# Performance work log

Hardware: AMD Instinct MI355X
Metric: run time of the kernel (lower is better)

Reference implementation:

```python
import jax, jax.numpy as jnp
import numpy as np

TOP_K = 2
EPS = 1e-6

def setup_inputs() -> dict:
    key = jax.random.key(0)
    ks = jax.random.split(key, 4)
    B, L, D, E, ED = 2, 2048, 2048, 8, 2048
    scale_gu = (6.0 / D) ** 0.5   # kaiming_uniform-ish bound
    scale_dn = (6.0 / ED) ** 0.5
    return {
        "x": jax.random.normal(ks[0], (B, L, D), jnp.float32),
        "router_scale": jnp.ones((D,), jnp.float32),
        "gate_w": jax.random.normal(ks[1], (D, E), jnp.float32) * (D ** -0.5),
        "gate_up": jax.random.uniform(ks[2], (E, D, 2 * ED), jnp.float32, -scale_gu, scale_gu),
        "down": jax.random.uniform(ks[3], (E, ED, D), jnp.float32, -scale_dn, scale_dn),
        "per_expert_scale": jnp.ones((E,), jnp.float32),
    }

def reference(x, router_scale, gate_w, gate_up, down, per_expert_scale):
    B, L, D = x.shape
    E = gate_up.shape[0]
    # --- Router: RMSNorm (no scale) * D^-0.5 * router_scale -> linear -> softmax -> topk -> renorm
    h = x * jax.lax.rsqrt(jnp.mean(x * x, axis=-1, keepdims=True) + EPS)
    h = h * (D ** -0.5) * router_scale
    logits = (h @ gate_w).astype(jnp.float32)            # [B,L,E]
    probs = jax.nn.softmax(logits, axis=-1)
    w, idx = jax.lax.top_k(probs, TOP_K)                 # [B,L,K]
    w = w / jnp.clip(jnp.sum(w, axis=-1, keepdims=True), 1e-12)
    w = w.astype(x.dtype)
    # --- Experts: dense compute over all experts, weighted combine by routing
    N = B * L
    xf = x.reshape(N, D)
    idxf = idx.reshape(N, TOP_K)
    wf = w.reshape(N, TOP_K)
    # combine[n,e] = sum_k wf[n,k] * (idxf[n,k]==e); top_k indices are distinct per token
    combine = jnp.zeros((N, E), x.dtype).at[jnp.arange(N)[:, None], idxf].add(wf)
    hh = jnp.einsum('nd,edf->nef', xf, gate_up)          # [N,E,2*ED]
    gate, up = jnp.split(hh, 2, axis=-1)
    act = jax.nn.gelu(gate, approximate=False) * up      # [N,E,ED]
    y = jnp.einsum('nef,efd->ned', act, down)            # [N,E,D]
    out = jnp.einsum('ne,ned->nd', combine * per_expert_scale, y)
    return out.reshape(B, L, D)
```

## Files before the change

### kernel.cpp

```cpp
#include <hip/hip_runtime.h>
#include <hip/hip_bf16.h>
#include <math.h>

#define NTOK 4096
#define DM   2048
#define NE   8
#define BM   128
#define BK   64

using f32x4  = float __attribute__((ext_vector_type(4)));
using bf16x8 = __bf16 __attribute__((ext_vector_type(8)));
using u32x4  = unsigned int __attribute__((ext_vector_type(4)));

__device__ __forceinline__ unsigned short bf16bits(float f){
  unsigned u = __builtin_bit_cast(unsigned, f);
  return (unsigned short)((u + 0x7fffu + ((u >> 16) & 1u)) >> 16);
}

__device__ __forceinline__ void load_lds16(const void* g, void* l){
  __builtin_amdgcn_global_load_lds(
      (const __attribute__((address_space(1))) unsigned int*)g,
      (__attribute__((address_space(3))) unsigned int*)l, 16, 0, 0);
}

__global__ __launch_bounds__(256) void router_kernel(
    const float* __restrict__ x, const float* __restrict__ rs,
    const float* __restrict__ gw, const float* __restrict__ pes,
    unsigned short* __restrict__ xbf, int* __restrict__ cnt,
    int* __restrict__ toklist, float* __restrict__ slotw)
{
  const int wv = threadIdx.x >> 6, l = threadIdx.x & 63;
  const int n = blockIdx.x * 4 + wv;
  const float* xr = x + (size_t)n * DM;
  unsigned short* xb = xbf + (size_t)n * DM;
  float ssq = 0.f;
  float lg[8] = {0,0,0,0,0,0,0,0};
  #pragma unroll
  for (int q = 0; q < 8; ++q){
    int c4 = l + 64 * q;
    float4 v = ((const float4*)xr)[c4];
    float4 r = ((const float4*)rs)[c4];
    ssq += v.x*v.x + v.y*v.y + v.z*v.z + v.w*v.w;
    ushort4 o; o.x = bf16bits(v.x); o.y = bf16bits(v.y); o.z = bf16bits(v.z); o.w = bf16bits(v.w);
    ((ushort4*)xb)[c4] = o;
    float xs0 = v.x*r.x, xs1 = v.y*r.y, xs2 = v.z*r.z, xs3 = v.w*r.w;
    const float4* gp = (const float4*)(gw + (size_t)c4 * 32);
    float4 ga, gb;
    ga = gp[0]; gb = gp[1];
    lg[0]+=xs0*ga.x; lg[1]+=xs0*ga.y; lg[2]+=xs0*ga.z; lg[3]+=xs0*ga.w;
    lg[4]+=xs0*gb.x; lg[5]+=xs0*gb.y; lg[6]+=xs0*gb.z; lg[7]+=xs0*gb.w;
    ga = gp[2]; gb = gp[3];
    lg[0]+=xs1*ga.x; lg[1]+=xs1*ga.y; lg[2]+=xs1*ga.z; lg[3]+=xs1*ga.w;
    lg[4]+=xs1*gb.x; lg[5]+=xs1*gb.y; lg[6]+=xs1*gb.z; lg[7]+=xs1*gb.w;
    ga = gp[4]; gb = gp[5];
    lg[0]+=xs2*ga.x; lg[1]+=xs2*ga.y; lg[2]+=xs2*ga.z; lg[3]+=xs2*ga.w;
    lg[4]+=xs2*gb.x; lg[5]+=xs2*gb.y; lg[6]+=xs2*gb.z; lg[7]+=xs2*gb.w;
    ga = gp[6]; gb = gp[7];
    lg[0]+=xs3*ga.x; lg[1]+=xs3*ga.y; lg[2]+=xs3*ga.z; lg[3]+=xs3*ga.w;
    lg[4]+=xs3*gb.x; lg[5]+=xs3*gb.y; lg[6]+=xs3*gb.z; lg[7]+=xs3*gb.w;
  }
  #pragma unroll
  for (int off = 32; off; off >>= 1){
    ssq += __shfl_xor(ssq, off, 64);
    #pragma unroll
    for (int e2 = 0; e2 < 8; ++e2) lg[e2] += __shfl_xor(lg[e2], off, 64);
  }
  if (l == 0){
    float c = rsqrtf(ssq * (1.0f/DM) + 1e-6f) * 0.022097086912079608f;
    float mx = -1e30f;
    #pragma unroll
    for (int e2 = 0; e2 < 8; ++e2){ lg[e2] *= c; mx = fmaxf(mx, lg[e2]); }
    float l0 = lg[0]; int i0 = 0;
    #pragma unroll
    for (int e2 = 1; e2 < 8; ++e2) if (lg[e2] > l0){ l0 = lg[e2]; i0 = e2; }
    int i1 = (i0 == 0) ? 1 : 0; float l1 = (i0 == 0) ? lg[1] : lg[0];
    #pragma unroll
    for (int e2 = 0; e2 < 8; ++e2){ if (e2 != i0 && lg[e2] > l1){ l1 = lg[e2]; i1 = e2; } }
    float p0 = expf(l0 - mx), p1 = expf(l1 - mx);
    float sw = fmaxf(p0 + p1, 1e-12f);
    float w0 = p0 / sw, w1 = p1 / sw;
    int s0 = atomicAdd(&cnt[i0], 1);
    toklist[i0 * NTOK + s0] = n;
    slotw[i0 * NTOK + s0] = w0 * pes[i0];
    int s1 = atomicAdd(&cnt[i1], 1);
    toklist[i1 * NTOK + s1] = n;
    slotw[i1 * NTOK + s1] = w1 * pes[i1];
  }
}

__global__ void scan_kernel(const int* __restrict__ cnt, int* __restrict__ basep){
  if (threadIdx.x == 0){
    int a = 0;
    for (int e = 0; e < NE; ++e){ basep[e] = a; a += cnt[e]; }
  }
}

__global__ __launch_bounds__(256) void conv_transpose_kernel(
    const float* __restrict__ W, unsigned short* __restrict__ Wt, int ncols)
{
  const int z = blockIdx.z;
  const float* src = W + (size_t)z * 2048 * ncols;
  unsigned short* dst = Wt + (size_t)z * ncols * 2048;
  const int n0 = blockIdx.x * 64, k0 = blockIdx.y * 64;
  __shared__ __align__(16) unsigned short t[64][72];
  const int tid = threadIdx.x;
  const int kl = tid >> 4;
  const int nl = (tid & 15) * 4;
  #pragma unroll
  for (int q = 0; q < 4; ++q){
    int k = kl + q * 16;
    float4 v = *(const float4*)(src + (size_t)(k0 + k) * ncols + n0 + nl);
    t[nl+0][k] = bf16bits(v.x);
    t[nl+1][k] = bf16bits(v.y);
    t[nl+2][k] = bf16bits(v.z);
    t[nl+3][k] = bf16bits(v.w);
  }
  __syncthreads();
  const int nr = tid >> 3;
  const int k8 = (tid & 7) * 8;
  #pragma unroll
  for (int q = 0; q < 2; ++q){
    int n = nr + q * 32;
    u32x4 v = *(const u32x4*)&t[n][k8];
    *(u32x4*)(dst + (size_t)(n0 + n) * 2048 + k0 + k8) = v;
  }
}

template<int MODE>
__global__ __launch_bounds__(256, MODE ? 3 : 2) void moe_gemm(
    const unsigned short* __restrict__ Abuf,
    const unsigned short* __restrict__ Wt,
    unsigned short* __restrict__ act,
    float* __restrict__ out,
    const int* __restrict__ cnt,
    const int* __restrict__ basep,
    const int* __restrict__ toklist,
    const float* __restrict__ slotw,
    int e0)
{
  constexpr int NH = (MODE == 0) ? 2 : 1;
  constexpr int BCOLS = NH * 128;
  const int z = blockIdx.z;
  const int e = e0 + z;
  const int ce = cnt[e];
  const int m0 = blockIdx.y * BM;
  if (m0 >= ce) return;
  const int fb = blockIdx.x * 128;
  const int tid = threadIdx.x;
  const int l = tid & 63;
  const int wv = tid >> 6;
  const int wr = wv >> 1, wc = wv & 1;
  const int baseE = basep[e];
  const size_t ncols = (MODE == 0) ? 4096 : 2048;
  const unsigned short* Wz = Wt + (size_t)z * ncols * 2048;

  __shared__ __align__(16) unsigned short As[BM * BK];
  __shared__ __align__(16) unsigned short Bs[BCOLS * BK];

  const unsigned short* asrc[4];
  #pragma unroll
  for (int q = 0; q < 4; ++q){
    int row = q * 32 + (tid >> 3);
    int g = (tid & 7) ^ (row & 7);
    long rs;
    if (MODE == 0) rs = toklist[e * NTOK + min(m0 + row, ce - 1)];
    else           rs = baseE + min(m0 + row, ce - 1);
    asrc[q] = Abuf + (size_t)rs * 2048 + g * 8;
  }
  const unsigned short* bsrc[NH * 4];
  #pragma unroll
  for (int q = 0; q < NH * 4; ++q){
    int col = q * 32 + (tid >> 3);
    int g = (tid & 7) ^ (col & 7);
    int n;
    if (MODE == 0) n = (col & 128) ? (2048 + fb + (col - 128)) : (fb + col);
    else           n = fb + col;
    bsrc[q] = Wz + (size_t)n * 2048 + g * 8;
  }

  f32x4 acc[NH][4][4];
  #pragma unroll
  for (int h = 0; h < NH; ++h)
    #pragma unroll
    for (int i = 0; i < 4; ++i)
      #pragma unroll
      for (int j = 0; j < 4; ++j)
        acc[h][i][j] = (f32x4){0.f, 0.f, 0.f, 0.f};

  const int aoff0 = (wr * 64 + (l & 15)) * BK;
  const int boff0 = (wc * 64 + (l & 15)) * BK;
  const int lsw = l & 7;
  const int lq = l >> 4;

  #pragma unroll 1
  for (int k0 = 0; k0 < 2048; k0 += BK){
    if (k0) __syncthreads();
    #pragma unroll
    for (int q = 0; q < 4; ++q)
      load_lds16(asrc[q] + k0, &As[q * 2048 + wv * 512]);
    #pragma unroll
    for (int q = 0; q < NH * 4; ++q)
      load_lds16(bsrc[q] + k0, &Bs[q * 2048 + wv * 512]);
    __syncthreads();
    #pragma unroll
    for (int kk = 0; kk < 2; ++kk){
      const int gsw = ((kk * 4 + lq) ^ lsw) * 8;
      bf16x8 af[4];
      #pragma unroll
      for (int mi = 0; mi < 4; ++mi)
        af[mi] = *(const bf16x8*)&As[aoff0 + mi * 16 * BK + gsw];
      #pragma unroll
      for (int h = 0; h < NH; ++h)
        #pragma unroll
        for (int ni = 0; ni < 4; ++ni){
          bf16x8 bfr = *(const bf16x8*)&Bs[boff0 + (h * 128 + ni * 16) * BK + gsw];
          #pragma unroll
          for (int mi = 0; mi < 4; ++mi)
            acc[h][mi][ni] = __builtin_amdgcn_mfma_f32_16x16x32_bf16(
                af[mi], bfr, acc[h][mi][ni], 0, 0, 0);
        }
    }
  }

  if (MODE == 0){
    const int fcol = fb + wc * 64 + (l & 15);
    #pragma unroll
    for (int mi = 0; mi < 4; ++mi)
      #pragma unroll
      for (int j = 0; j < 4; ++j){
        int s = m0 + wr * 64 + mi * 16 + lq * 4 + j;
        if (s < ce){
          size_t rowb = (size_t)(baseE + s) * 2048 + fcol;
          #pragma unroll
          for (int ni = 0; ni < 4; ++ni){
            float g = acc[0][mi][ni][j];
            float u = acc[1][mi][ni][j];
            float a = 0.5f * g * (1.0f + erff(g * 0.70710678118654752f)) * u;
            act[rowb + ni * 16] = bf16bits(a);
          }
        }
      }
  } else {
    #pragma unroll
    for (int mi = 0; mi < 4; ++mi)
      #pragma unroll
      for (int j = 0; j < 4; ++j){
        int s = m0 + wr * 64 + mi * 16 + lq * 4 + j;
        if (s < ce){
          int tokn = toklist[e * NTOK + s];
          float wgt = slotw[e * NTOK + s];
          float* orow = out + (size_t)tokn * 2048 + fb + wc * 64 + (l & 15);
          #pragma unroll
          for (int ni = 0; ni < 4; ++ni)
            atomicAdd(&orow[ni * 16], wgt * acc[0][mi][ni][j]);
        }
      }
  }
}

extern "C" void kernel_launch(void* const* d_in, const int* in_sizes, int n_in,
                              void* d_out, int out_size, void* d_ws, size_t ws_size,
                              hipStream_t stream)
{
  const float* x   = (const float*)d_in[0];
  const float* rs  = (const float*)d_in[1];
  const float* gw  = (const float*)d_in[2];
  const float* w1  = (const float*)d_in[3];
  const float* w2  = (const float*)d_in[4];
  const float* pes = (const float*)d_in[5];
  float* out = (float*)d_out;

  char* ws = (char*)d_ws;
  int*   cnt     = (int*)ws;
  int*   basep   = (int*)(ws + 64);
  int*   toklist = (int*)(ws + 256);
  float* slotw   = (float*)(ws + 256 + (size_t)NE * NTOK * 4);
  unsigned short* xbf = (unsigned short*)(ws + 256 + 2 * (size_t)NE * NTOK * 4);
  unsigned short* act = xbf + (size_t)NTOK * DM;
  unsigned short* wtb = act + (size_t)2 * NTOK * DM;

  const size_t fixed = (size_t)((char*)wtb - ws);
  const size_t per_e = (size_t)4096 * 2048 * 2;
  int EG = NE;
  while (EG > 1 && fixed + (size_t)EG * per_e > ws_size) EG >>= 1;

  hipMemsetAsync(d_out, 0, (size_t)out_size * sizeof(float), stream);
  hipMemsetAsync(cnt, 0, 64, stream);
  router_kernel<<<NTOK / 4, 256, 0, stream>>>(x, rs, gw, pes, xbf, cnt, toklist, slotw);
  scan_kernel<<<1, 64, 0, stream>>>(cnt, basep);

  for (int g = 0; g < NE; g += EG){
    conv_transpose_kernel<<<dim3(64, 32, EG), 256, 0, stream>>>(
        w1 + (size_t)g * 2048 * 4096, wtb, 4096);
    moe_gemm<0><<<dim3(16, 32, EG), 256, 0, stream>>>(
        xbf, wtb, act, out, cnt, basep, toklist, slotw, g);
  }
  for (int g = 0; g < NE; g += EG){
    conv_transpose_kernel<<<dim3(32, 32, EG), 256, 0, stream>>>(
        w2 + (size_t)g * 2048 * 2048, wtb, 2048);
    moe_gemm<1><<<dim3(16, 32, EG), 256, 0, stream>>>(
        act, wtb, act, out, cnt, basep, toklist, slotw, g);
  }
}
```

Baseline: 540.5 us.

## Rewrite MoE GEMM as 256x256 tile, 8-wave, 4-stage LDS pipeline

The MoE expert GEMM moves from 128-row tiles and 256 threads to 256x256 output tiles with 512 threads (8 waves). It uses a 4-buffer LDS ring with BK=32, prefetching three stages ahead via global_load_lds, with split barriers and s_setprio around the MFMA bursts. Gate and up columns are interleaved per 32-column group so each wave holds both halves for the GELU epilogue. The aim is to hide global-load latency and raise operand reuse per LDS byte, at the cost of higher register pressure, fewer blocks and more wasted rows when an expert's token count is not a multiple of 256.

```diff
diff --git a/kernel.cpp b/kernel.cpp
--- a/kernel.cpp
+++ b/kernel.cpp
@@ -5,8 +5,10 @@
 #define NTOK 4096
 #define DM   2048
 #define NE   8
-#define BM   128
-#define BK   64
+#define BK2  32
+#define NT   64
+#define TILE_BYTES 32768
+#define B_OFF      16384
 
 using f32x4  = float __attribute__((ext_vector_type(4)));
 using bf16x8 = __bf16 __attribute__((ext_vector_type(8)));
@@ -127,7 +129,7 @@
 }
 
 template<int MODE>
-__global__ __launch_bounds__(256, MODE ? 3 : 2) void moe_gemm(
+__global__ __launch_bounds__(512, 2) void moe_gemm(
     const unsigned short* __restrict__ Abuf,
     const unsigned short* __restrict__ Wt,
     unsigned short* __restrict__ act,
@@ -138,121 +140,148 @@
     const float* __restrict__ slotw,
     int e0)
 {
-  constexpr int NH = (MODE == 0) ? 2 : 1;
-  constexpr int BCOLS = NH * 128;
-  const int z = blockIdx.z;
-  const int e = e0 + z;
+  const int z = blockIdx.z, e = e0 + z;
   const int ce = cnt[e];
-  const int m0 = blockIdx.y * BM;
+  const int m0 = blockIdx.y * 256;
   if (m0 >= ce) return;
-  const int fb = blockIdx.x * 128;
+  const int fb = blockIdx.x * (MODE == 0 ? 128 : 256);
   const int tid = threadIdx.x;
   const int l = tid & 63;
   const int wv = tid >> 6;
-  const int wr = wv >> 1, wc = wv & 1;
+  const int wr = wv >> 2;
+  const int wc = wv & 3;
   const int baseE = basep[e];
   const size_t ncols = (MODE == 0) ? 4096 : 2048;
   const unsigned short* Wz = Wt + (size_t)z * ncols * 2048;
 
-  __shared__ __align__(16) unsigned short As[BM * BK];
-  __shared__ __align__(16) unsigned short Bs[BCOLS * BK];
-
-  const unsigned short* asrc[4];
-  #pragma unroll
-  for (int q = 0; q < 4; ++q){
-    int row = q * 32 + (tid >> 3);
-    int g = (tid & 7) ^ (row & 7);
-    long rs;
-    if (MODE == 0) rs = toklist[e * NTOK + min(m0 + row, ce - 1)];
-    else           rs = baseE + min(m0 + row, ce - 1);
-    asrc[q] = Abuf + (size_t)rs * 2048 + g * 8;
-  }
-  const unsigned short* bsrc[NH * 4];
-  #pragma unroll
-  for (int q = 0; q < NH * 4; ++q){
-    int col = q * 32 + (tid >> 3);
-    int g = (tid & 7) ^ (col & 7);
+  __shared__ __align__(16) unsigned short smem[4 * TILE_BYTES / 2];
+
+  const unsigned short* asrc[2];
+  #pragma unroll
+  for (int q = 0; q < 2; ++q){
+    int r = q * 128 + (tid >> 2);
+    int g = (tid & 3) ^ ((r >> 1) & 3);
+    long rsrc;
+    if (MODE == 0) rsrc = toklist[e * NTOK + min(m0 + r, ce - 1)];
+    else           rsrc = baseE + min(m0 + r, ce - 1);
+    asrc[q] = Abuf + (size_t)rsrc * 2048 + g * 8;
+  }
+  const unsigned short* bsrc[2];
+  #pragma unroll
+  for (int q = 0; q < 2; ++q){
+    int col = q * 128 + (tid >> 2);
+    int g = (tid & 3) ^ ((col >> 1) & 3);
     int n;
-    if (MODE == 0) n = (col & 128) ? (2048 + fb + (col - 128)) : (fb + col);
-    else           n = fb + col;
+    if (MODE == 0){ int sub = col & 63; n = fb + (col >> 6) * 32 + (sub & 31) + ((sub & 32) ? 2048 : 0); }
+    else n = fb + col;
     bsrc[q] = Wz + (size_t)n * 2048 + g * 8;
   }
-
-  f32x4 acc[NH][4][4];
-  #pragma unroll
-  for (int h = 0; h < NH; ++h)
-    #pragma unroll
-    for (int i = 0; i < 4; ++i)
-      #pragma unroll
-      for (int j = 0; j < 4; ++j)
-        acc[h][i][j] = (f32x4){0.f, 0.f, 0.f, 0.f};
-
-  const int aoff0 = (wr * 64 + (l & 15)) * BK;
-  const int boff0 = (wc * 64 + (l & 15)) * BK;
-  const int lsw = l & 7;
-  const int lq = l >> 4;
+  const int ldst = tid * 16;
+
+  const int kq = l >> 4;
+  const int swz = (kq ^ (((l & 15) >> 1) & 3)) * 16;
+  const int abase = (wr * 128 + (l & 15)) * 64 + swz;
+  const int bbase = B_OFF + (wc * 64 + (l & 15)) * 64 + swz;
+
+  f32x4 acc[8][4];
+  #pragma unroll
+  for (int i = 0; i < 8; ++i)
+    #pragma unroll
+    for (int j = 0; j < 4; ++j)
+      acc[i][j] = (f32x4){0.f, 0.f, 0.f, 0.f};
+
+  auto stage_a = [&](int buf, int st){
+    char* base = (char*)smem + buf * TILE_BYTES;
+    load_lds16(asrc[0] + st * BK2, base + ldst);
+    load_lds16(asrc[1] + st * BK2, base + 8192 + ldst);
+  };
+  auto stage_b = [&](int buf, int st){
+    char* base = (char*)smem + buf * TILE_BYTES + B_OFF;
+    load_lds16(bsrc[0] + st * BK2, base + ldst);
+    load_lds16(bsrc[1] + st * BK2, base + 8192 + ldst);
+  };
+
+  stage_a(0, 0); stage_b(0, 0);
+  stage_a(1, 1); stage_b(1, 1);
+  stage_a(2, 2); stage_b(2, 2);
+  asm volatile("s_waitcnt vmcnt(8)" ::: "memory");
+  __builtin_amdgcn_s_barrier();
+  asm volatile("" ::: "memory");
 
   #pragma unroll 1
-  for (int k0 = 0; k0 < 2048; k0 += BK){
-    if (k0) __syncthreads();
-    #pragma unroll
-    for (int q = 0; q < 4; ++q)
-      load_lds16(asrc[q] + k0, &As[q * 2048 + wv * 512]);
-    #pragma unroll
-    for (int q = 0; q < NH * 4; ++q)
-      load_lds16(bsrc[q] + k0, &Bs[q * 2048 + wv * 512]);
-    __syncthreads();
-    #pragma unroll
-    for (int kk = 0; kk < 2; ++kk){
-      const int gsw = ((kk * 4 + lq) ^ lsw) * 8;
-      bf16x8 af[4];
+  for (int kt = 0; kt < NT; ++kt){
+    const char* C = (const char*)smem + (kt & 3) * TILE_BYTES;
+    const int sb = (kt + 3) & 3;
+    const int st = min(kt + 3, NT - 1);
+    bf16x8 af[4], bfr[4];
+    #pragma unroll
+    for (int ni = 0; ni < 4; ++ni) bfr[ni] = *(const bf16x8*)(C + bbase + ni * 1024);
+    #pragma unroll
+    for (int mi = 0; mi < 4; ++mi) af[mi] = *(const bf16x8*)(C + abase + mi * 1024);
+    stage_a(sb, st);
+    asm volatile("" ::: "memory");
+    __builtin_amdgcn_s_barrier();
+    asm volatile("" ::: "memory");
+    __builtin_amdgcn_s_setprio(1);
+    #pragma unroll
+    for (int ni = 0; ni < 4; ++ni)
       #pragma unroll
       for (int mi = 0; mi < 4; ++mi)
-        af[mi] = *(const bf16x8*)&As[aoff0 + mi * 16 * BK + gsw];
+        acc[mi][ni] = __builtin_amdgcn_mfma_f32_16x16x32_bf16(af[mi], bfr[ni], acc[mi][ni], 0, 0, 0);
+    __builtin_amdgcn_s_setprio(0);
+    asm volatile("" ::: "memory");
+    __builtin_amdgcn_s_barrier();
+    asm volatile("" ::: "memory");
+    #pragma unroll
+    for (int mi = 0; mi < 4; ++mi) af[mi] = *(const bf16x8*)(C + abase + (mi + 4) * 1024);
+    stage_b(sb, st);
+    asm volatile("" ::: "memory");
+    __builtin_amdgcn_s_barrier();
+    asm volatile("" ::: "memory");
+    __builtin_amdgcn_s_setprio(1);
+    #pragma unroll
+    for (int ni = 0; ni < 4; ++ni)
       #pragma unroll
-      for (int h = 0; h < NH; ++h)
-        #pragma unroll
-        for (int ni = 0; ni < 4; ++ni){
-          bf16x8 bfr = *(const bf16x8*)&Bs[boff0 + (h * 128 + ni * 16) * BK + gsw];
-          #pragma unroll
-          for (int mi = 0; mi < 4; ++mi)
-            acc[h][mi][ni] = __builtin_amdgcn_mfma_f32_16x16x32_bf16(
-                af[mi], bfr, acc[h][mi][ni], 0, 0, 0);
-        }
-    }
-  }
-
+      for (int mi = 0; mi < 4; ++mi)
+        acc[mi + 4][ni] = __builtin_amdgcn_mfma_f32_16x16x32_bf16(af[mi], bfr[ni], acc[mi + 4][ni], 0, 0, 0);
+    __builtin_amdgcn_s_setprio(0);
+    asm volatile("s_waitcnt vmcnt(8)" ::: "memory");
+    __builtin_amdgcn_s_barrier();
+    asm volatile("" ::: "memory");
+  }
+  asm volatile("s_waitcnt vmcnt(0)" ::: "memory");
+
+  const int lq4 = (l >> 4) * 4;
   if (MODE == 0){
-    const int fcol = fb + wc * 64 + (l & 15);
-    #pragma unroll
-    for (int mi = 0; mi < 4; ++mi)
+    #pragma unroll
+    for (int mi = 0; mi < 8; ++mi)
       #pragma unroll
       for (int j = 0; j < 4; ++j){
-        int s = m0 + wr * 64 + mi * 16 + lq * 4 + j;
+        int s = m0 + wr * 128 + mi * 16 + lq4 + j;
         if (s < ce){
-          size_t rowb = (size_t)(baseE + s) * 2048 + fcol;
+          size_t rowb = (size_t)(baseE + s) * 2048;
           #pragma unroll
-          for (int ni = 0; ni < 4; ++ni){
-            float g = acc[0][mi][ni][j];
-            float u = acc[1][mi][ni][j];
+          for (int p = 0; p < 2; ++p){
+            float g = acc[mi][p][j];
+            float u = acc[mi][p + 2][j];
             float a = 0.5f * g * (1.0f + erff(g * 0.70710678118654752f)) * u;
-            act[rowb + ni * 16] = bf16bits(a);
+            act[rowb + fb + wc * 32 + p * 16 + (l & 15)] = bf16bits(a);
           }
         }
       }
   } else {
     #pragma unroll
-    for (int mi = 0; mi < 4; ++mi)
+    for (int mi = 0; mi < 8; ++mi)
       #pragma unroll
       for (int j = 0; j < 4; ++j){
-        int s = m0 + wr * 64 + mi * 16 + lq * 4 + j;
+        int s = m0 + wr * 128 + mi * 16 + lq4 + j;
         if (s < ce){
           int tokn = toklist[e * NTOK + s];
           float wgt = slotw[e * NTOK + s];
           float* orow = out + (size_t)tokn * 2048 + fb + wc * 64 + (l & 15);
           #pragma unroll
           for (int ni = 0; ni < 4; ++ni)
-            atomicAdd(&orow[ni * 16], wgt * acc[0][mi][ni][j]);
+            atomicAdd(&orow[ni * 16], wgt * acc[mi][ni][j]);
         }
       }
   }
@@ -292,13 +321,13 @@
   for (int g = 0; g < NE; g += EG){
     conv_transpose_kernel<<<dim3(64, 32, EG), 256, 0, stream>>>(
         w1 + (size_t)g * 2048 * 4096, wtb, 4096);
-    moe_gemm<0><<<dim3(16, 32, EG), 256, 0, stream>>>(
+    moe_gemm<0><<<dim3(16, 16, EG), 512, 0, stream>>>(
         xbf, wtb, act, out, cnt, basep, toklist, slotw, g);
   }
   for (int g = 0; g < NE; g += EG){
     conv_transpose_kernel<<<dim3(32, 32, EG), 256, 0, stream>>>(
         w2 + (size_t)g * 2048 * 2048, wtb, 2048);
-    moe_gemm<1><<<dim3(16, 32, EG), 256, 0, stream>>>(
+    moe_gemm<1><<<dim3(8, 16, EG), 512, 0, stream>>>(
         act, wtb, act, out, cnt, basep, toklist, slotw, g);
   }
 }
```

New measurement: 564.9 us. +4.5%, slower.

## Unfuse GELU from gate-up GEMM to shrink tiles and raise occupancy

Applied to the files above, without the earlier changes.

The gate-up GEMM now computes one 128-column tile per block instead of paired gate/up tiles, using half the accumulators and LDS. This allows launch bounds of 4 blocks per SM for both GEMM modes. The pre-activation is written to a new bf16 buffer, and a separate elementwise kernel applies GELU times up. The trade is an extra round trip of the full hidden tensor through memory and one extra launch. Expert grouping now uses as many experts as fit in the workspace, not a power of two.

```diff
diff --git a/kernel.cpp b/kernel.cpp
--- a/kernel.cpp
+++ b/kernel.cpp
@@ -5,7 +5,6 @@
 #define NTOK 4096
 #define DM   2048
 #define NE   8
-#define BM   128
 #define BK   64
 
 using f32x4  = float __attribute__((ext_vector_type(4)));
@@ -16,6 +15,9 @@
   unsigned u = __builtin_bit_cast(unsigned, f);
   return (unsigned short)((u + 0x7fffu + ((u >> 16) & 1u)) >> 16);
 }
+
+__device__ __forceinline__ float bfhi(unsigned u){ return __builtin_bit_cast(float, u & 0xffff0000u); }
+__device__ __forceinline__ float bflo(unsigned u){ return __builtin_bit_cast(float, u << 16); }
 
 __device__ __forceinline__ void load_lds16(const void* g, void* l){
   __builtin_amdgcn_global_load_lds(
@@ -127,10 +129,10 @@
 }
 
 template<int MODE>
-__global__ __launch_bounds__(256, MODE ? 3 : 2) void moe_gemm(
+__global__ __launch_bounds__(256, 4) void moe_gemm(
     const unsigned short* __restrict__ Abuf,
     const unsigned short* __restrict__ Wt,
-    unsigned short* __restrict__ act,
+    unsigned short* __restrict__ hh,
     float* __restrict__ out,
     const int* __restrict__ cnt,
     const int* __restrict__ basep,
@@ -138,12 +140,9 @@
     const float* __restrict__ slotw,
     int e0)
 {
-  constexpr int NH = (MODE == 0) ? 2 : 1;
-  constexpr int BCOLS = NH * 128;
-  const int z = blockIdx.z;
-  const int e = e0 + z;
+  const int z = blockIdx.z, e = e0 + z;
   const int ce = cnt[e];
-  const int m0 = blockIdx.y * BM;
+  const int m0 = blockIdx.y * 128;
   if (m0 >= ce) return;
   const int fb = blockIdx.x * 128;
   const int tid = threadIdx.x;
@@ -154,10 +153,11 @@
   const size_t ncols = (MODE == 0) ? 4096 : 2048;
   const unsigned short* Wz = Wt + (size_t)z * ncols * 2048;
 
-  __shared__ __align__(16) unsigned short As[BM * BK];
-  __shared__ __align__(16) unsigned short Bs[BCOLS * BK];
+  __shared__ __align__(16) unsigned short As[128 * BK];
+  __shared__ __align__(16) unsigned short Bs[128 * BK];
 
   const unsigned short* asrc[4];
+  const unsigned short* bsrc[4];
   #pragma unroll
   for (int q = 0; q < 4; ++q){
     int row = q * 32 + (tid >> 3);
@@ -166,26 +166,15 @@
     if (MODE == 0) rs = toklist[e * NTOK + min(m0 + row, ce - 1)];
     else           rs = baseE + min(m0 + row, ce - 1);
     asrc[q] = Abuf + (size_t)rs * 2048 + g * 8;
-  }
-  const unsigned short* bsrc[NH * 4];
-  #pragma unroll
-  for (int q = 0; q < NH * 4; ++q){
-    int col = q * 32 + (tid >> 3);
-    int g = (tid & 7) ^ (col & 7);
-    int n;
-    if (MODE == 0) n = (col & 128) ? (2048 + fb + (col - 128)) : (fb + col);
-    else           n = fb + col;
-    bsrc[q] = Wz + (size_t)n * 2048 + g * 8;
-  }
-
-  f32x4 acc[NH][4][4];
-  #pragma unroll
-  for (int h = 0; h < NH; ++h)
-    #pragma unroll
-    for (int i = 0; i < 4; ++i)
-      #pragma unroll
-      for (int j = 0; j < 4; ++j)
-        acc[h][i][j] = (f32x4){0.f, 0.f, 0.f, 0.f};
+    bsrc[q] = Wz + (size_t)(fb + row) * 2048 + g * 8;
+  }
+
+  f32x4 acc[4][4];
+  #pragma unroll
+  for (int i = 0; i < 4; ++i)
+    #pragma unroll
+    for (int j = 0; j < 4; ++j)
+      acc[i][j] = (f32x4){0.f, 0.f, 0.f, 0.f};
 
   const int aoff0 = (wr * 64 + (l & 15)) * BK;
   const int boff0 = (wc * 64 + (l & 15)) * BK;
@@ -199,7 +188,7 @@
     for (int q = 0; q < 4; ++q)
       load_lds16(asrc[q] + k0, &As[q * 2048 + wv * 512]);
     #pragma unroll
-    for (int q = 0; q < NH * 4; ++q)
+    for (int q = 0; q < 4; ++q)
       load_lds16(bsrc[q] + k0, &Bs[q * 2048 + wv * 512]);
     __syncthreads();
     #pragma unroll
@@ -210,34 +199,29 @@
       for (int mi = 0; mi < 4; ++mi)
         af[mi] = *(const bf16x8*)&As[aoff0 + mi * 16 * BK + gsw];
       #pragma unroll
-      for (int h = 0; h < NH; ++h)
+      for (int ni = 0; ni < 4; ++ni){
+        bf16x8 bfr = *(const bf16x8*)&Bs[boff0 + ni * 16 * BK + gsw];
         #pragma unroll
-        for (int ni = 0; ni < 4; ++ni){
-          bf16x8 bfr = *(const bf16x8*)&Bs[boff0 + (h * 128 + ni * 16) * BK + gsw];
-          #pragma unroll
-          for (int mi = 0; mi < 4; ++mi)
-            acc[h][mi][ni] = __builtin_amdgcn_mfma_f32_16x16x32_bf16(
-                af[mi], bfr, acc[h][mi][ni], 0, 0, 0);
-        }
+        for (int mi = 0; mi < 4; ++mi)
+          acc[mi][ni] = __builtin_amdgcn_mfma_f32_16x16x32_bf16(
+              af[mi], bfr, acc[mi][ni], 0, 0, 0);
+      }
     }
   }
 
+  const int lq4 = (l >> 4) * 4;
   if (MODE == 0){
     const int fcol = fb + wc * 64 + (l & 15);
     #pragma unroll
     for (int mi = 0; mi < 4; ++mi)
       #pragma unroll
       for (int j = 0; j < 4; ++j){
-        int s = m0 + wr * 64 + mi * 16 + lq * 4 + j;
+        int s = m0 + wr * 64 + mi * 16 + lq4 + j;
         if (s < ce){
-          size_t rowb = (size_t)(baseE + s) * 2048 + fcol;
+          size_t rowb = (size_t)(baseE + s) * 4096 + fcol;
           #pragma unroll
-          for (int ni = 0; ni < 4; ++ni){
-            float g = acc[0][mi][ni][j];
-            float u = acc[1][mi][ni][j];
-            float a = 0.5f * g * (1.0f + erff(g * 0.70710678118654752f)) * u;
-            act[rowb + ni * 16] = bf16bits(a);
-          }
+          for (int ni = 0; ni < 4; ++ni)
+            hh[rowb + ni * 16] = bf16bits(acc[mi][ni][j]);
         }
       }
   } else {
@@ -245,17 +229,38 @@
     for (int mi = 0; mi < 4; ++mi)
       #pragma unroll
       for (int j = 0; j < 4; ++j){
-        int s = m0 + wr * 64 + mi * 16 + lq * 4 + j;
+        int s = m0 + wr * 64 + mi * 16 + lq4 + j;
         if (s < ce){
           int tokn = toklist[e * NTOK + s];
           float wgt = slotw[e * NTOK + s];
           float* orow = out + (size_t)tokn * 2048 + fb + wc * 64 + (l & 15);
           #pragma unroll
           for (int ni = 0; ni < 4; ++ni)
-            atomicAdd(&orow[ni * 16], wgt * acc[0][mi][ni][j]);
+            atomicAdd(&orow[ni * 16], wgt * acc[mi][ni][j]);
         }
       }
   }
+}
+
+__global__ __launch_bounds__(256) void gelu_mul_kernel(
+    const unsigned short* __restrict__ hh, unsigned short* __restrict__ act)
+{
+  const int s = blockIdx.x;
+  const int t = threadIdx.x;
+  const unsigned short* gp = hh + (size_t)s * 4096 + t * 8;
+  u32x4 gv = *(const u32x4*)gp;
+  u32x4 uv = *(const u32x4*)(gp + 2048);
+  unsigned short r[8];
+  #pragma unroll
+  for (int i = 0; i < 4; ++i){
+    float g0 = bflo(gv[i]), g1 = bfhi(gv[i]);
+    float u0 = bflo(uv[i]), u1 = bfhi(uv[i]);
+    float a0 = 0.5f * g0 * (1.0f + erff(g0 * 0.70710678118654752f)) * u0;
+    float a1 = 0.5f * g1 * (1.0f + erff(g1 * 0.70710678118654752f)) * u1;
+    r[2*i]   = bf16bits(a0);
+    r[2*i+1] = bf16bits(a1);
+  }
+  *(u32x4*)(act + (size_t)s * 2048 + t * 8) = *(u32x4*)r;
 }
 
 extern "C" void kernel_launch(void* const* d_in, const int* in_sizes, int n_in,
@@ -271,34 +276,39 @@
   float* out = (float*)d_out;
 
   char* ws = (char*)d_ws;
-  int*   cnt     = (int*)ws;
-  int*   basep   = (int*)(ws + 64);
-  int*   toklist = (int*)(ws + 256);
-  float* slotw   = (float*)(ws + 256 + (size_t)NE * NTOK * 4);
-  unsigned short* xbf = (unsigned short*)(ws + 256 + 2 * (size_t)NE * NTOK * 4);
-  unsigned short* act = xbf + (size_t)NTOK * DM;
-  unsigned short* wtb = act + (size_t)2 * NTOK * DM;
+  int*   cnt      = (int*)ws;
+  int*   basep    = (int*)(ws + 64);
+  int*   toklist  = (int*)(ws + 256);
+  float* slotw    = (float*)(ws + 256 + (size_t)NE * NTOK * 4);
+  unsigned short* xbf  = (unsigned short*)(ws + 256 + 2 * (size_t)NE * NTOK * 4);
+  unsigned short* act  = xbf + (size_t)NTOK * DM;
+  unsigned short* hh   = act + (size_t)2 * NTOK * DM;
+  unsigned short* wtb  = hh + (size_t)2 * NTOK * 4096;
 
   const size_t fixed = (size_t)((char*)wtb - ws);
   const size_t per_e = (size_t)4096 * 2048 * 2;
-  int EG = NE;
-  while (EG > 1 && fixed + (size_t)EG * per_e > ws_size) EG >>= 1;
-
-  hipMemsetAsync(d_out, 0, (size_t)out_size * sizeof(float), stream);
+  int EG = (int)((ws_size > fixed) ? ((ws_size - fixed) / per_e) : 0);
+  if (EG < 1) EG = 1;
+  if (EG > NE) EG = NE;
+
+  hipMemsetAsync(out, 0, (size_t)out_size * sizeof(float), stream);
   hipMemsetAsync(cnt, 0, 64, stream);
   router_kernel<<<NTOK / 4, 256, 0, stream>>>(x, rs, gw, pes, xbf, cnt, toklist, slotw);
   scan_kernel<<<1, 64, 0, stream>>>(cnt, basep);
 
   for (int g = 0; g < NE; g += EG){
-    conv_transpose_kernel<<<dim3(64, 32, EG), 256, 0, stream>>>(
+    int gg = min(EG, NE - g);
+    conv_transpose_kernel<<<dim3(64, 32, gg), 256, 0, stream>>>(
         w1 + (size_t)g * 2048 * 4096, wtb, 4096);
-    moe_gemm<0><<<dim3(16, 32, EG), 256, 0, stream>>>(
-        xbf, wtb, act, out, cnt, basep, toklist, slotw, g);
-  }
+    moe_gemm<0><<<dim3(32, 32, gg), 256, 0, stream>>>(
+        xbf, wtb, hh, out, cnt, basep, toklist, slotw, g);
+  }
+  gelu_mul_kernel<<<2 * NTOK, 256, 0, stream>>>(hh, act);
   for (int g = 0; g < NE; g += EG){
-    conv_transpose_kernel<<<dim3(32, 32, EG), 256, 0, stream>>>(
+    int gg = min(EG, NE - g);
+    conv_transpose_kernel<<<dim3(32, 32, gg), 256, 0, stream>>>(
         w2 + (size_t)g * 2048 * 2048, wtb, 2048);
-    moe_gemm<1><<<dim3(16, 32, EG), 256, 0, stream>>>(
-        act, wtb, act, out, cnt, basep, toklist, slotw, g);
-  }
-}
+    moe_gemm<1><<<dim3(16, 32, gg), 256, 0, stream>>>(
+        act, wtb, hh, out, cnt, basep, toklist, slotw, g);
+  }
+}
```

New measurement: 527.6 us. 2.4% less time.
